# Performance work log

Hardware: AMD Instinct MI355X
Metric: run time of the kernel (lower is better)

Reference implementation:

```python
import jax, jax.numpy as jnp
import numpy as np

S = 4          # num_segments
T = 4096       # frames
D = 1024       # input_size == output_size
HEADS = 1
FREQ = 10000.0
DH = D // HEADS     # per-head width = 1024
TB = T // S         # block height = 1024
WB = DH // S        # block width  = 256


def _abs_pos(tb, d, freq):
    # Matches getAbsolutePosition: AP[p, 2i] = sin(p / freq^(2i/d)), AP[p, 2i+1] = cos(same).
    pos = jnp.arange(tb, dtype=jnp.float32)[:, None]          # [tb,1]
    i = jnp.arange(tb // 2, dtype=jnp.float32)[None, :]       # [1,tb//2]
    ang = pos / jnp.power(jnp.float32(freq), 2.0 * i / d)     # [tb,tb//2]
    ap = jnp.zeros((tb, tb), jnp.float32)
    return ap.at[:, 0::2].set(jnp.sin(ang)).at[:, 1::2].set(jnp.cos(ang))


def setup_inputs() -> dict:
    key = jax.random.key(0)
    ks = jax.random.split(key, 6)
    x = jax.random.normal(ks[0], (T, D), jnp.float32)
    Wq = jax.random.normal(ks[1], (HEADS, DH, D), jnp.float32) * 0.02
    Wk = jax.random.normal(ks[2], (HEADS, DH, D), jnp.float32) * 0.02
    Wv = jax.random.normal(ks[3], (HEADS, DH, D), jnp.float32) * 0.02
    Wout = jax.random.normal(ks[4], (D, D), jnp.float32) * 0.02
    Wout2 = jax.random.normal(ks[5], (WB, WB + 2), jnp.float32) * 0.05
    return {"x": x, "Wq": Wq, "Wk": Wk, "Wv": Wv, "Wout": Wout, "Wout2": Wout2}


def _forward(x, Wq, Wk, Wv, Wout, Wout2):
    # diversity = 1 - cosine similarity (F.normalize p=2 along dim=1)
    xu = x / jnp.maximum(jnp.linalg.norm(x, axis=1, keepdims=True), 1e-12)
    div = 1.0 - xu @ xu.T                                     # [T,T]

    Q = jnp.einsum('ti,hdi->htd', x, Wq)                      # [h,T,DH]
    K = jnp.einsum('ti,hdi->htd', x, Wk)
    V = jnp.einsum('ti,hdi->htd', x, Wv)

    def blk(A):  # [h,T,DH] -> [h,S*S,TB,WB], block (i,j) row-major as in local_x/local_y
        return A.reshape(-1, S, TB, S, WB).transpose(0, 1, 3, 2, 4).reshape(-1, S * S, TB, WB)

    qb, kb, vb = blk(Q), blk(K), blk(V)
    # diversity uses the diagonal row-block for every column-block j of row i
    drow = jnp.stack([div[i * TB:(i + 1) * TB, i * TB:(i + 1) * TB] for i in range(S)], 0)  # [S,TB,TB]
    db = jnp.repeat(drow, S, axis=0)[None]                    # [1,S*S,TB,TB]

    sim = jnp.einsum('hbqc,hbkc->hbqk', qb, kb) + _abs_pos(TB, D, FREQ)  # [h,S*S,TB,TB]
    attw = jax.nn.softmax(sim, axis=-1)
    # normalized row entropy, then L1-normalized (F.normalize p=1)
    ent = -(attw * jax.nn.log_softmax(sim, axis=-1)).sum(-1) / jnp.log(jnp.float32(TB))  # [h,S*S,TB]
    ent = ent / jnp.maximum(jnp.abs(ent).sum(-1, keepdims=True), 1e-12)

    dep = (db * attw).sum(-1) / db.sum(-1)                    # [h,S*S,TB]
    att_win = attw + dep[:, :, None, :] * attw                # dep_factor rows are identical
    ctx = jnp.einsum('hbqk,hbkc->hbqc', att_win, vb)          # [h,S*S,TB,WB]

    chars = jax.lax.stop_gradient(jnp.stack([ent, dep], axis=-1))  # [h,S*S,TB,2] (detach)
    y = jnp.concatenate([ctx, chars], axis=-1) @ Wout2.T      # [h,S*S,TB,WB]

    # reassemble grid of blocks back to [h,T,DH], concat heads, final projection
    y = y.reshape(-1, S, S, TB, WB).transpose(0, 1, 3, 2, 4).reshape(-1, T, DH)
    y = y.transpose(1, 0, 2).reshape(T, HEADS * DH)
    return y @ Wout.T                                         # [T,D]


def reference(x, Wq, Wk, Wv, Wout, Wout2):
    return _forward(x, Wq, Wk, Wv, Wout, Wout2)
```

## Files before the change

kernel.cpp:

```cpp
#include <hip/hip_runtime.h>
#include <hip/hip_bf16.h>

#define TT 4096
#define DD 1024
#define TBB 1024
#define WBB 256

typedef __attribute__((ext_vector_type(8))) _Float16 half8;
typedef __attribute__((ext_vector_type(4))) _Float16 half4;
typedef __attribute__((ext_vector_type(16))) float f32x16;

__device__ __forceinline__ unsigned short f2h(float v) {
  _Float16 h = (_Float16)v;
  return *reinterpret_cast<unsigned short*>(&h);
}
__device__ __forceinline__ float h2f(unsigned short u) {
  _Float16 h = *reinterpret_cast<_Float16*>(&u);
  return (float)h;
}

__device__ __forceinline__ void gl_lds16(const unsigned short* g, unsigned short* l) {
  __builtin_amdgcn_global_load_lds(
      (const __attribute__((address_space(1))) void*)(unsigned long long)(g),
      (__attribute__((address_space(3))) void*)(unsigned long long)(l),
      16, 0, 0);
}

__device__ __forceinline__ float waveSum(float v) {
#pragma unroll
  for (int o = 32; o > 0; o >>= 1) v += __shfl_down(v, o, 64);
  return v;
}
__device__ __forceinline__ float waveMax(float v) {
#pragma unroll
  for (int o = 32; o > 0; o >>= 1) v = fmaxf(v, __shfl_down(v, o, 64));
  return v;
}

template <int EPI, typename OutT>
__global__ __launch_bounds__(256) void gemm_bt(
    const unsigned short* __restrict__ A, const unsigned short* __restrict__ B,
    OutT* __restrict__ C,
    int K, int lda, int ldb, int ldc,
    int zbase, int zdiv,
    long sAi, long sAj, long sBi, long sBj, long sCi, long sCj,
    long sAz, long sBz, long sCz,
    const float* __restrict__ e0, const float* __restrict__ e1,
    const float* __restrict__ e2, const float* __restrict__ e3)
{
  __shared__ __align__(16) unsigned short lA[2][4096];
  __shared__ __align__(16) unsigned short lB[2][4096];

  const int z = blockIdx.z, gz = zbase + z;
  const int zi = gz / zdiv, zj = gz - zi * zdiv;
  const unsigned short* Ab = A + (long)zi * sAi + (long)zj * sAj + (long)z * sAz;
  const unsigned short* Bb = B + (long)zi * sBi + (long)zj * sBj + (long)z * sBz;
  const long offC = (long)zi * sCi + (long)zj * sCj + (long)z * sCz;

  const int m0 = blockIdx.y * 128, n0 = blockIdx.x * 128;
  const int tid = threadIdx.x, wave = tid >> 6, lane = tid & 63;
  const int wm = (wave >> 1) * 64, wn = (wave & 1) * 64;
  const int srow = lane >> 2;
  const int scol = (((lane & 3) ^ ((srow >> 1) & 3))) * 8;
  const int l31 = lane & 31, khi = lane >> 5;
  const int sw2 = (l31 >> 1) & 3;

  f32x16 acc[2][2] = {};

  for (int k0 = 0; k0 < K; k0 += 64) {
#pragma unroll
    for (int h = 0; h < 2; ++h)
#pragma unroll
      for (int t = 0; t < 2; ++t) {
        const int r = wave * 32 + t * 16 + srow;
        gl_lds16(Ab + (long)(m0 + r) * lda + (k0 + h * 32 + scol), &lA[h][wave * 1024 + t * 512]);
        gl_lds16(Bb + (long)(n0 + r) * ldb + (k0 + h * 32 + scol), &lB[h][wave * 1024 + t * 512]);
      }
    __syncthreads();

    half8 af[2][4], bfr[2][4];
#pragma unroll
    for (int mi = 0; mi < 2; ++mi)
#pragma unroll
      for (int ks = 0; ks < 4; ++ks)
        af[mi][ks] = *(const half8*)&lA[ks >> 1][(wm + mi * 32 + l31) * 32 + ((((ks & 1) * 2 + khi) ^ sw2) * 8)];
#pragma unroll
    for (int ni = 0; ni < 2; ++ni)
#pragma unroll
      for (int ks = 0; ks < 4; ++ks)
        bfr[ni][ks] = *(const half8*)&lB[ks >> 1][(wn + ni * 32 + l31) * 32 + ((((ks & 1) * 2 + khi) ^ sw2) * 8)];

#pragma unroll
    for (int ks = 0; ks < 4; ++ks)
#pragma unroll
      for (int mi = 0; mi < 2; ++mi)
#pragma unroll
        for (int ni = 0; ni < 2; ++ni)
          acc[mi][ni] = __builtin_amdgcn_mfma_f32_32x32x16_f16(af[mi][ks], bfr[ni][ks], acc[mi][ni], 0, 0, 0);
    __syncthreads();
  }

  OutT* Cb = C + offC;
#pragma unroll
  for (int mi = 0; mi < 2; ++mi)
#pragma unroll
    for (int ni = 0; ni < 2; ++ni)
#pragma unroll
      for (int r = 0; r < 16; ++r) {
        const int row = m0 + wm + mi * 32 + khi * 4 + (r & 3) + 8 * (r >> 2);
        const int col = n0 + wn + ni * 32 + l31;
        float v = acc[mi][ni][r];
        const long ci = (long)row * ldc + col;
        if constexpr (sizeof(OutT) == 2) {
          Cb[ci] = (OutT)f2h(v);
        } else {
          Cb[ci] = v;
        }
      }
}

template <int EPI, typename OutT>
__global__ __launch_bounds__(256) void gemm_s(
    const unsigned short* __restrict__ A, const unsigned short* __restrict__ B,
    OutT* __restrict__ C,
    int K, int lda, int ldb, int ldc,
    int zbase, int zdiv,
    long sAi, long sAj, long sBi, long sBj, long sCi, long sCj,
    long sAz, long sBz, long sCz,
    const float* __restrict__ e0, const float* __restrict__ e1,
    const float* __restrict__ e2, const float* __restrict__ e3)
{
  __shared__ __align__(16) unsigned short lA[2][2048];
  __shared__ __align__(16) unsigned short lB[2][2048];

  const int z = blockIdx.z, gz = zbase + z;
  const int zi = gz / zdiv, zj = gz - zi * zdiv;
  const unsigned short* Ab = A + (long)zi * sAi + (long)zj * sAj + (long)z * sAz;
  const unsigned short* Bb = B + (long)zi * sBi + (long)zj * sBj + (long)z * sBz;
  const long offC = (long)zi * sCi + (long)zj * sCj + (long)z * sCz;

  const int m0 = blockIdx.y * 64, n0 = blockIdx.x * 64;
  const int tid = threadIdx.x, wave = tid >> 6, lane = tid & 63;
  const int wm = (wave >> 1) * 32, wn = (wave & 1) * 32;
  const int srow = lane >> 2;
  const int grow = wave * 16 + srow;
  const int scol = (((lane & 3) ^ ((grow >> 1) & 3))) * 8;
  const int l31 = lane & 31, khi = lane >> 5;
  const int sw2 = (l31 >> 1) & 3;

  f32x16 acc = {};

  for (int k0 = 0; k0 < K; k0 += 64) {
#pragma unroll
    for (int h = 0; h < 2; ++h) {
      gl_lds16(Ab + (long)(m0 + grow) * lda + (k0 + h * 32 + scol), &lA[h][wave * 512]);
      gl_lds16(Bb + (long)(n0 + grow) * ldb + (k0 + h * 32 + scol), &lB[h][wave * 512]);
    }
    __syncthreads();

    half8 af[4], bfr[4];
#pragma unroll
    for (int ks = 0; ks < 4; ++ks) {
      af[ks] = *(const half8*)&lA[ks >> 1][(wm + l31) * 32 + ((((ks & 1) * 2 + khi) ^ sw2) * 8)];
      bfr[ks] = *(const half8*)&lB[ks >> 1][(wn + l31) * 32 + ((((ks & 1) * 2 + khi) ^ sw2) * 8)];
    }
#pragma unroll
    for (int ks = 0; ks < 4; ++ks)
      acc = __builtin_amdgcn_mfma_f32_32x32x16_f16(af[ks], bfr[ks], acc, 0, 0, 0);
    __syncthreads();
  }

  OutT* Cb = C + offC;
#pragma unroll
  for (int r = 0; r < 16; ++r) {
    const int row = m0 + wm + khi * 4 + (r & 3) + 8 * (r >> 2);
    const int col = n0 + wn + l31;
    float v = acc[r];
    if constexpr (EPI == 1) v = 1.0f - v;
    if constexpr (EPI == 3)
      v += e0[(long)gz * 1024 + row] * e2[col] + e1[(long)gz * 1024 + row] * e3[col];
    const long ci = (long)row * ldc + col;
    if constexpr (sizeof(OutT) == 2) {
      Cb[ci] = (OutT)f2h(v);
    } else {
      Cb[ci] = v;
    }
  }
}

__global__ __launch_bounds__(256) void sim_gemm(
    const unsigned short* __restrict__ A, const unsigned short* __restrict__ B,
    unsigned short* __restrict__ C,
    const unsigned short* __restrict__ APh)
{
  __shared__ __align__(16) unsigned short lA[2][4096];
  __shared__ __align__(16) unsigned short lB[2][4096];

  const int gz = blockIdx.z;
  const int zi = gz >> 2, zj = gz & 3;
  const unsigned short* Ab = A + (long)zi * (TBB * DD) + zj * WBB;
  const unsigned short* Bb = B + (long)zi * (TBB * DD) + zj * WBB;
  unsigned short* Cb = C + (long)gz * TBB * TBB;

  const int m0 = blockIdx.y * 128, n0 = blockIdx.x * 128;
  const int tid = threadIdx.x, wave = tid >> 6, lane = tid & 63;
  const int wm = (wave >> 1) * 64, wn = (wave & 1) * 64;
  const int srow = lane >> 2;
  const int scol = ((lane & 3) ^ ((srow >> 1) & 3)) * 8;
  const int l31 = lane & 31, khi = lane >> 5;
  const int sw2 = (l31 >> 1) & 3;

  f32x16 acc[2][2] = {};

  for (int k0 = 0; k0 < WBB; k0 += 64) {
#pragma unroll
    for (int h = 0; h < 2; ++h)
#pragma unroll
      for (int t = 0; t < 2; ++t) {
        const int r = wave * 32 + t * 16 + srow;
        gl_lds16(Ab + (long)(m0 + r) * DD + (k0 + h * 32 + scol), &lA[h][wave * 1024 + t * 512]);
        gl_lds16(Bb + (long)(n0 + r) * DD + (k0 + h * 32 + scol), &lB[h][wave * 1024 + t * 512]);
      }
    __syncthreads();

    half8 af[2][4], bfr[2][4];
#pragma unroll
    for (int mi = 0; mi < 2; ++mi)
#pragma unroll
      for (int ks = 0; ks < 4; ++ks)
        af[mi][ks] = *(const half8*)&lA[ks >> 1][(wm + mi * 32 + l31) * 32 + ((((ks & 1) * 2 + khi) ^ sw2) * 8)];
#pragma unroll
    for (int ni = 0; ni < 2; ++ni)
#pragma unroll
      for (int ks = 0; ks < 4; ++ks)
        bfr[ni][ks] = *(const half8*)&lB[ks >> 1][(wn + ni * 32 + l31) * 32 + ((((ks & 1) * 2 + khi) ^ sw2) * 8)];

#pragma unroll
    for (int ks = 0; ks < 4; ++ks)
#pragma unroll
      for (int mi = 0; mi < 2; ++mi)
#pragma unroll
        for (int ni = 0; ni < 2; ++ni)
          acc[mi][ni] = __builtin_amdgcn_mfma_f32_32x32x16_f16(af[mi][ks], bfr[ni][ks], acc[mi][ni], 0, 0, 0);
    __syncthreads();
  }

#pragma unroll
  for (int mi = 0; mi < 2; ++mi)
#pragma unroll
    for (int ni = 0; ni < 2; ++ni)
#pragma unroll
      for (int r = 0; r < 16; ++r) {
        const int row = m0 + wm + mi * 32 + khi * 4 + (r & 3) + 8 * (r >> 2);
        const int col = n0 + wn + ni * 32 + l31;
        Cb[(long)row * TBB + col] = f2h(acc[mi][ni][r] + h2f(APh[(long)row * 1024 + col]));
      }
}

__global__ __launch_bounds__(256) void ctx_gemm_s(
    const unsigned short* __restrict__ wpre, const float* __restrict__ dep,
    const unsigned short* __restrict__ Vt, unsigned short* __restrict__ ctx)
{
  __shared__ __align__(16) unsigned short lA[2][2048];
  __shared__ __align__(16) unsigned short lB[2][2048];
  __shared__ __align__(16) unsigned short sDepH[1024];

  const int gz = blockIdx.z, zi = gz >> 2, zj = gz & 3;
  const int m0 = blockIdx.y * 64, n0 = blockIdx.x * 64;
  const int tid = threadIdx.x, wave = tid >> 6, lane = tid & 63;
  const int wm = (wave >> 1) * 32, wn = (wave & 1) * 32;
  const int srow = lane >> 2;
  const int grow = wave * 16 + srow;
  const int scol = ((lane & 3) ^ ((grow >> 1) & 3)) * 8;
  const int l31 = lane & 31, khi = lane >> 5;
  const int sw2 = (l31 >> 1) & 3;

#pragma unroll
  for (int p = 0; p < 4; ++p)
    sDepH[tid + p * 256] = f2h(1.f + dep[(long)gz * 1024 + tid + p * 256]);
  __syncthreads();

  const unsigned short* Ab = wpre + (long)gz * TBB * TBB;
  const unsigned short* Bb = Vt + (long)(zj * 256) * TT + (long)zi * 1024;

  f32x16 acc = {};

  for (int k0 = 0; k0 < 1024; k0 += 64) {
#pragma unroll
    for (int h = 0; h < 2; ++h)
      gl_lds16(Bb + (long)(n0 + grow) * TT + (k0 + h * 32 + scol), &lB[h][wave * 512]);
#pragma unroll
    for (int h = 0; h < 2; ++h)
#pragma unroll
      for (int p = 0; p < 2; ++p) {
        const int idx = p * 1024 + tid * 4;
        const int row = idx >> 5, col = idx & 31;
        ushort4 wv = *(const ushort4*)(Ab + (long)(m0 + row) * 1024 + k0 + h * 32 + col);
        const half4 dv = *(const half4*)&sDepH[k0 + h * 32 + col];
        half4 pv = *(half4*)&wv * dv;
        const int pcol = (((col >> 3) ^ ((row >> 1) & 3)) << 3) | (col & 7);
        *(half4*)&lA[h][row * 32 + pcol] = pv;
      }
    __syncthreads();

    half8 af[4], bfr[4];
#pragma unroll
    for (int ks = 0; ks < 4; ++ks) {
      af[ks] = *(const half8*)&lA[ks >> 1][(wm + l31) * 32 + ((((ks & 1) * 2 + khi) ^ sw2) * 8)];
      bfr[ks] = *(const half8*)&lB[ks >> 1][(wn + l31) * 32 + ((((ks & 1) * 2 + khi) ^ sw2) * 8)];
    }
#pragma unroll
    for (int ks = 0; ks < 4; ++ks)
      acc = __builtin_amdgcn_mfma_f32_32x32x16_f16(af[ks], bfr[ks], acc, 0, 0, 0);
    __syncthreads();
  }

  unsigned short* Cb = ctx + (long)gz * TBB * WBB;
#pragma unroll
  for (int r = 0; r < 16; ++r) {
    const int row = m0 + wm + khi * 4 + (r & 3) + 8 * (r >> 2);
    const int col = n0 + wn + l31;
    Cb[(long)row * WBB + col] = f2h(acc[r]);
  }
}

__global__ __launch_bounds__(256) void prepx_kernel(
    const float* __restrict__ x, unsigned short* __restrict__ xh,
    unsigned short* __restrict__ xu)
{
  const int t = blockIdx.x, tid = threadIdx.x;
  const float4 v = *((const float4*)(x + (long)t * DD) + tid);
  float ss = v.x * v.x + v.y * v.y + v.z * v.z + v.w * v.w;
  ss = waveSum(ss);
  __shared__ float red[4];
  if ((tid & 63) == 0) red[tid >> 6] = ss;
  __syncthreads();
  const float tot = red[0] + red[1] + red[2] + red[3];
  const float inv = 1.f / fmaxf(sqrtf(tot), 1e-12f);
  ushort4 h, u;
  h.x = f2h(v.x); h.y = f2h(v.y); h.z = f2h(v.z); h.w = f2h(v.w);
  u.x = f2h(v.x * inv); u.y = f2h(v.y * inv); u.z = f2h(v.z * inv); u.w = f2h(v.w * inv);
  *((ushort4*)(xh + (long)t * DD) + tid) = h;
  *((ushort4*)(xu + (long)t * DD) + tid) = u;
}

__global__ __launch_bounds__(256) void castw_kernel(
    const float* __restrict__ Wq, const float* __restrict__ Wk, const float* __restrict__ Wv,
    unsigned short* __restrict__ o)
{
  const long idx4 = ((long)blockIdx.x * 256 + threadIdx.x) * 4;
  const int which = (int)(idx4 >> 20);
  const long loc = idx4 & ((1L << 20) - 1);
  const float* src = (which == 0) ? Wq : ((which == 1) ? Wk : Wv);
  const float4 v = *(const float4*)(src + loc);
  ushort4 h;
  h.x = f2h(v.x); h.y = f2h(v.y); h.z = f2h(v.z); h.w = f2h(v.w);
  *(ushort4*)(o + idx4) = h;
}

__global__ __launch_bounds__(256) void castp_kernel(const float* __restrict__ src,
                                                    unsigned short* __restrict__ dst)
{
  const long idx4 = ((long)blockIdx.x * 256 + threadIdx.x) * 4;
  const float4 v = *(const float4*)(src + idx4);
  ushort4 h;
  h.x = f2h(v.x); h.y = f2h(v.y); h.z = f2h(v.z); h.w = f2h(v.w);
  *(ushort4*)(dst + idx4) = h;
}

__global__ __launch_bounds__(256) void packw2_kernel(
    const float* __restrict__ W2, unsigned short* __restrict__ W2B,
    float* __restrict__ Ecol, float* __restrict__ Dcol)
{
  const int c = blockIdx.x, j = threadIdx.x;
  W2B[c * 256 + j] = f2h(W2[c * 258 + j]);
  if (j == 0) {
    Ecol[c] = W2[c * 258 + 256];
    Dcol[c] = W2[c * 258 + 257];
  }
}

__global__ __launch_bounds__(256) void ap_kernel(unsigned short* __restrict__ APh)
{
  const int p = blockIdx.x, tid = threadIdx.x;
#pragma unroll
  for (int t = 0; t < 4; ++t) {
    const int col = tid + t * 256;
    const int i = col >> 1;
    const float e = (2.0f * (float)i) / 1024.0f;
    const float ang = (float)p / powf(10000.0f, e);
    APh[(long)p * 1024 + col] = f2h((col & 1) ? cosf(ang) : sinf(ang));
  }
}

__global__ __launch_bounds__(256) void transpose_kernel(
    const unsigned short* __restrict__ V, unsigned short* __restrict__ Vt)
{
  __shared__ unsigned short tile[32][33];
  const int tx = threadIdx.x & 31, ty = threadIdx.x >> 5;
  const int c0 = blockIdx.x * 32;
  const int r0 = blockIdx.y * 32;
#pragma unroll
  for (int rr = ty; rr < 32; rr += 8)
    tile[rr][tx] = V[(long)(r0 + rr) * DD + c0 + tx];
  __syncthreads();
#pragma unroll
  for (int rr = ty; rr < 32; rr += 8)
    Vt[(long)(c0 + rr) * TT + r0 + tx] = tile[tx][rr];
}

__global__ __launch_bounds__(256) void stats_kernel(
    const unsigned short* __restrict__ sim, const unsigned short* __restrict__ divb,
    float* __restrict__ dep, float* __restrict__ ent,
    unsigned short* __restrict__ wpre)
{
  const int q = blockIdx.x, gz = blockIdx.y, bi = gz >> 2;
  const int tid = threadIdx.x;
  const unsigned short* srow = sim + ((long)gz * TBB + q) * TBB;
  const unsigned short* drow = divb + ((long)bi * TBB + q) * TBB;
  const ushort4 sv = ((const ushort4*)srow)[tid];
  const ushort4 dv = ((const ushort4*)drow)[tid];
  float s[4] = {h2f(sv.x), h2f(sv.y), h2f(sv.z), h2f(sv.w)};
  float d[4] = {h2f(dv.x), h2f(dv.y), h2f(dv.z), h2f(dv.w)};
  float m = fmaxf(fmaxf(s[0], s[1]), fmaxf(s[2], s[3]));
  m = waveMax(m);
  __shared__ float red[4];
  if ((tid & 63) == 0) red[tid >> 6] = m;
  __syncthreads();
  m = fmaxf(fmaxf(red[0], red[1]), fmaxf(red[2], red[3]));
  float e[4];
  float l = 0.f, ss = 0.f, dn = 0.f, ds = 0.f;
#pragma unroll
  for (int p = 0; p < 4; ++p) {
    e[p] = expf(s[p] - m);
    l += e[p]; ss += e[p] * s[p]; dn += e[p] * d[p]; ds += d[p];
  }
  l = waveSum(l); ss = waveSum(ss); dn = waveSum(dn); ds = waveSum(ds);
  __shared__ float r2[16];
  if ((tid & 63) == 0) {
    const int w = tid >> 6;
    r2[w] = l; r2[4 + w] = ss; r2[8 + w] = dn; r2[12 + w] = ds;
  }
  __syncthreads();
  const float L = r2[0] + r2[1] + r2[2] + r2[3];
  const float Li = 1.f / L;
  ushort4 wq;
  wq.x = f2h(e[0] * Li); wq.y = f2h(e[1] * Li);
  wq.z = f2h(e[2] * Li); wq.w = f2h(e[3] * Li);
  ((ushort4*)(wpre + ((long)gz * TBB + q) * TBB))[tid] = wq;
  if (tid == 0) {
    const float SS = r2[4] + r2[5] + r2[6] + r2[7];
    const float DN = r2[8] + r2[9] + r2[10] + r2[11];
    const float DS = r2[12] + r2[13] + r2[14] + r2[15];
    const long o = (long)gz * TBB + q;
    dep[o] = (DN * Li) / DS;
    ent[o] = (m + logf(L) - SS * Li) * 0.14426950408889634f;
  }
}

__global__ __launch_bounds__(256) void entnorm_kernel(float* __restrict__ ent)
{
  const int gz = blockIdx.x, tid = threadIdx.x;
  float s = 0.f;
#pragma unroll
  for (int p = 0; p < 4; ++p) s += fabsf(ent[(long)gz * TBB + tid + p * 256]);
  s = waveSum(s);
  __shared__ float red[4];
  if ((tid & 63) == 0) red[tid >> 6] = s;
  __syncthreads();
  const float scale = 1.f / fmaxf(red[0] + red[1] + red[2] + red[3], 1e-12f);
#pragma unroll
  for (int p = 0; p < 4; ++p) ent[(long)gz * TBB + tid + p * 256] *= scale;
}

extern "C" void kernel_launch(void* const* d_in, const int* in_sizes, int n_in,
                              void* d_out, int out_size, void* d_ws, size_t ws_size,
                              hipStream_t stream)
{
  const float* x  = (const float*)d_in[0];
  const float* Wq = (const float*)d_in[1];
  const float* Wk = (const float*)d_in[2];
  const float* Wv = (const float*)d_in[3];
  const float* Wo = (const float*)d_in[4];
  const float* W2 = (const float*)d_in[5];

  char* ws = (char*)d_ws;
  size_t off = 0;
  auto take = [&](size_t bytes) -> void* {
    void* p = ws + off;
    off += (bytes + 255) & ~(size_t)255;
    return p;
  };
  unsigned short* QKV = (unsigned short*)take((size_t)3 * TT * DD * 2);
  unsigned short* xh  = (unsigned short*)take((size_t)TT * DD * 2);
  unsigned short* xu  = (unsigned short*)take((size_t)TT * DD * 2);
  unsigned short* Wh  = (unsigned short*)take((size_t)3 * DD * DD * 2);
  unsigned short* WoB = (unsigned short*)take((size_t)DD * DD * 2);
  unsigned short* W2B = (unsigned short*)take((size_t)256 * 256 * 2);
  float* Ecol = (float*)take(256 * 4);
  float* Dcol = (float*)take(256 * 4);
  unsigned short* APh = (unsigned short*)take((size_t)TBB * TBB * 2);
  unsigned short* divb = (unsigned short*)take((size_t)4 * TBB * TBB * 2);
  unsigned short* Vt = (unsigned short*)take((size_t)DD * TT * 2);
  unsigned short* simh = (unsigned short*)take((size_t)16 * TBB * TBB * 2);
  unsigned short* wpre = (unsigned short*)take((size_t)16 * TBB * TBB * 2);
  float* depb = (float*)take((size_t)16 * TBB * 4);
  float* entb = (float*)take((size_t)16 * TBB * 4);
  unsigned short* ctx = (unsigned short*)take((size_t)16 * TBB * WBB * 2);
  unsigned short* Y = (unsigned short*)take((size_t)TT * DD * 2);
  (void)ws_size; (void)in_sizes; (void)n_in; (void)out_size;

  prepx_kernel<<<TT, 256, 0, stream>>>(x, xh, xu);
  castw_kernel<<<(3 * DD * DD) / 1024, 256, 0, stream>>>(Wq, Wk, Wv, Wh);
  castp_kernel<<<(DD * DD) / 1024, 256, 0, stream>>>(Wo, WoB);
  packw2_kernel<<<256, 256, 0, stream>>>(W2, W2B, Ecol, Dcol);
  ap_kernel<<<TBB, 256, 0, stream>>>(APh);

  gemm_bt<0, unsigned short><<<dim3(DD / 128, TT / 128, 3), 256, 0, stream>>>(
      xh, Wh, QKV,
      DD, DD, DD, DD, 0, 1,
      0, 0, (long)DD * DD, 0, (long)TT * DD, 0,
      0, 0, 0, nullptr, nullptr, nullptr, nullptr);

  transpose_kernel<<<dim3(DD / 32, TT / 32), 256, 0, stream>>>(QKV + (size_t)2 * TT * DD, Vt);

  gemm_s<1, unsigned short><<<dim3(16, 16, 4), 256, 0, stream>>>(
      xu, xu, divb,
      DD, DD, DD, TBB, 0, 1,
      (long)TBB * DD, 0, (long)TBB * DD, 0, (long)TBB * TBB, 0,
      0, 0, 0, nullptr, nullptr, nullptr, nullptr);

  const unsigned short* Qh = QKV;
  const unsigned short* Kh = QKV + (size_t)TT * DD;

  sim_gemm<<<dim3(8, 8, 16), 256, 0, stream>>>(Qh, Kh, simh, APh);

  stats_kernel<<<dim3(TBB, 16), 256, 0, stream>>>(simh, divb, depb, entb, wpre);
  entnorm_kernel<<<16, 256, 0, stream>>>(entb);

  ctx_gemm_s<<<dim3(4, 16, 16), 256, 0, stream>>>(wpre, depb, Vt, ctx);

  gemm_s<3, unsigned short><<<dim3(4, 16, 16), 256, 0, stream>>>(
      ctx, W2B, Y,
      WBB, WBB, WBB, DD, 0, 4,
      (long)4 * TBB * WBB, (long)TBB * WBB, 0, 0, (long)TBB * DD, (long)WBB,
      0, 0, 0, entb, depb, Ecol, Dcol);

  gemm_s<0, float><<<dim3(16, 64, 1), 256, 0, stream>>>(
      Y, WoB, (float*)d_out,
      DD, DD, DD, DD, 0, 1,
      0, 0, 0, 0, 0, 0,
      0, 0, 0, nullptr, nullptr, nullptr, nullptr);
}
```

Baseline: 271.4 us.

## Recompute softmax probabilities in ctx GEMM and fold entropy normalization into stats

The stats kernel stops writing a normalized fp16 probability matrix. It now writes a per-row log-sum-exp offset, and the context GEMM recomputes exp(sim - B) while loading its A tile. This removes a 32 MB write and its later re-read, at the cost of extra exp work inside the GEMM prologue. The stats kernel is also reworked to handle one row per wave with xor shuffles and no shared memory. The entropy L1 normalization kernel is dropped: sums are accumulated by atomics and the scale is applied in the Wout2 epilogue. Separately, the two weight-cast kernels are merged into one.

```diff
diff --git a/kernel.cpp b/kernel.cpp
--- a/kernel.cpp
+++ b/kernel.cpp
@@ -31,9 +31,14 @@
   for (int o = 32; o > 0; o >>= 1) v += __shfl_down(v, o, 64);
   return v;
 }
-__device__ __forceinline__ float waveMax(float v) {
-#pragma unroll
-  for (int o = 32; o > 0; o >>= 1) v = fmaxf(v, __shfl_down(v, o, 64));
+__device__ __forceinline__ float bSum(float v) {
+#pragma unroll
+  for (int o = 32; o > 0; o >>= 1) v += __shfl_xor(v, o, 64);
+  return v;
+}
+__device__ __forceinline__ float bMax(float v) {
+#pragma unroll
+  for (int o = 32; o > 0; o >>= 1) v = fmaxf(v, __shfl_xor(v, o, 64));
   return v;
 }
 
@@ -46,7 +51,8 @@
     long sAi, long sAj, long sBi, long sBj, long sCi, long sCj,
     long sAz, long sBz, long sCz,
     const float* __restrict__ e0, const float* __restrict__ e1,
-    const float* __restrict__ e2, const float* __restrict__ e3)
+    const float* __restrict__ e2, const float* __restrict__ e3,
+    const float* __restrict__ e4)
 {
   __shared__ __align__(16) unsigned short lA[2][4096];
   __shared__ __align__(16) unsigned short lB[2][4096];
@@ -128,7 +134,8 @@
     long sAi, long sAj, long sBi, long sBj, long sCi, long sCj,
     long sAz, long sBz, long sCz,
     const float* __restrict__ e0, const float* __restrict__ e1,
-    const float* __restrict__ e2, const float* __restrict__ e3)
+    const float* __restrict__ e2, const float* __restrict__ e3,
+    const float* __restrict__ e4)
 {
   __shared__ __align__(16) unsigned short lA[2][2048];
   __shared__ __align__(16) unsigned short lB[2][2048];
@@ -148,6 +155,9 @@
   const int l31 = lane & 31, khi = lane >> 5;
   const int sw2 = (l31 >> 1) & 3;
 
+  float esc = 0.f;
+  if constexpr (EPI == 3) esc = 1.f / fmaxf(e4[gz], 1e-12f);
+
   f32x16 acc = {};
 
   for (int k0 = 0; k0 < K; k0 += 64) {
@@ -178,7 +188,7 @@
     float v = acc[r];
     if constexpr (EPI == 1) v = 1.0f - v;
     if constexpr (EPI == 3)
-      v += e0[(long)gz * 1024 + row] * e2[col] + e1[(long)gz * 1024 + row] * e3[col];
+      v += e0[(long)gz * 1024 + row] * esc * e2[col] + e1[(long)gz * 1024 + row] * e3[col];
     const long ci = (long)row * ldc + col;
     if constexpr (sizeof(OutT) == 2) {
       Cb[ci] = (OutT)f2h(v);
@@ -258,7 +268,8 @@
 }
 
 __global__ __launch_bounds__(256) void ctx_gemm_s(
-    const unsigned short* __restrict__ wpre, const float* __restrict__ dep,
+    const unsigned short* __restrict__ simh, const float* __restrict__ dep,
+    const float* __restrict__ Brow,
     const unsigned short* __restrict__ Vt, unsigned short* __restrict__ ctx)
 {
   __shared__ __align__(16) unsigned short lA[2][2048];
@@ -280,7 +291,10 @@
     sDepH[tid + p * 256] = f2h(1.f + dep[(long)gz * 1024 + tid + p * 256]);
   __syncthreads();
 
-  const unsigned short* Ab = wpre + (long)gz * TBB * TBB;
+  const float B0 = Brow[(long)gz * 1024 + m0 + (tid >> 3)];
+  const float B1 = Brow[(long)gz * 1024 + m0 + 32 + (tid >> 3)];
+
+  const unsigned short* Ab = simh + (long)gz * TBB * TBB;
   const unsigned short* Bb = Vt + (long)(zj * 256) * TT + (long)zi * 1024;
 
   f32x16 acc = {};
@@ -295,9 +309,15 @@
       for (int p = 0; p < 2; ++p) {
         const int idx = p * 1024 + tid * 4;
         const int row = idx >> 5, col = idx & 31;
-        ushort4 wv = *(const ushort4*)(Ab + (long)(m0 + row) * 1024 + k0 + h * 32 + col);
+        const ushort4 wv = *(const ushort4*)(Ab + (long)(m0 + row) * 1024 + k0 + h * 32 + col);
+        const float Bp = p ? B1 : B0;
+        half4 ev;
+        ev.x = (_Float16)exp2f(fmaf(h2f(wv.x), 1.4426950408889634f, -Bp));
+        ev.y = (_Float16)exp2f(fmaf(h2f(wv.y), 1.4426950408889634f, -Bp));
+        ev.z = (_Float16)exp2f(fmaf(h2f(wv.z), 1.4426950408889634f, -Bp));
+        ev.w = (_Float16)exp2f(fmaf(h2f(wv.w), 1.4426950408889634f, -Bp));
         const half4 dv = *(const half4*)&sDepH[k0 + h * 32 + col];
-        half4 pv = *(half4*)&wv * dv;
+        half4 pv = ev * dv;
         const int pcol = (((col >> 3) ^ ((row >> 1) & 3)) << 3) | (col & 7);
         *(half4*)&lA[h][row * 32 + pcol] = pv;
       }
@@ -344,33 +364,26 @@
   *((ushort4*)(xu + (long)t * DD) + tid) = u;
 }
 
-__global__ __launch_bounds__(256) void castw_kernel(
-    const float* __restrict__ Wq, const float* __restrict__ Wk, const float* __restrict__ Wv,
-    unsigned short* __restrict__ o)
+__global__ __launch_bounds__(256) void castall_kernel(
+    const float* __restrict__ Wq, const float* __restrict__ Wk,
+    const float* __restrict__ Wv, const float* __restrict__ Wo,
+    unsigned short* __restrict__ Wh, unsigned short* __restrict__ WoB)
 {
   const long idx4 = ((long)blockIdx.x * 256 + threadIdx.x) * 4;
   const int which = (int)(idx4 >> 20);
   const long loc = idx4 & ((1L << 20) - 1);
-  const float* src = (which == 0) ? Wq : ((which == 1) ? Wk : Wv);
+  const float* src = (which == 0) ? Wq : ((which == 1) ? Wk : ((which == 2) ? Wv : Wo));
+  unsigned short* dst = (which < 3) ? (Wh + idx4) : (WoB + loc);
   const float4 v = *(const float4*)(src + loc);
   ushort4 h;
   h.x = f2h(v.x); h.y = f2h(v.y); h.z = f2h(v.z); h.w = f2h(v.w);
-  *(ushort4*)(o + idx4) = h;
-}
-
-__global__ __launch_bounds__(256) void castp_kernel(const float* __restrict__ src,
-                                                    unsigned short* __restrict__ dst)
-{
-  const long idx4 = ((long)blockIdx.x * 256 + threadIdx.x) * 4;
-  const float4 v = *(const float4*)(src + idx4);
-  ushort4 h;
-  h.x = f2h(v.x); h.y = f2h(v.y); h.z = f2h(v.z); h.w = f2h(v.w);
-  *(ushort4*)(dst + idx4) = h;
+  *(ushort4*)dst = h;
 }
 
 __global__ __launch_bounds__(256) void packw2_kernel(
     const float* __restrict__ W2, unsigned short* __restrict__ W2B,
-    float* __restrict__ Ecol, float* __restrict__ Dcol)
+    float* __restrict__ Ecol, float* __restrict__ Dcol,
+    float* __restrict__ entsum)
 {
   const int c = blockIdx.x, j = threadIdx.x;
   W2B[c * 256 + j] = f2h(W2[c * 258 + j]);
@@ -378,6 +391,7 @@
     Ecol[c] = W2[c * 258 + 256];
     Dcol[c] = W2[c * 258 + 257];
   }
+  if (c == 0 && j < 16) entsum[j] = 0.f;
 }
 
 __global__ __launch_bounds__(256) void ap_kernel(unsigned short* __restrict__ APh)
@@ -388,7 +402,7 @@
     const int col = tid + t * 256;
     const int i = col >> 1;
     const float e = (2.0f * (float)i) / 1024.0f;
-    const float ang = (float)p / powf(10000.0f, e);
+    const float ang = (float)p * exp2f(e * -13.287712379549449f);
     APh[(long)p * 1024 + col] = f2h((col & 1) ? cosf(ang) : sinf(ang));
   }
 }
@@ -412,65 +426,45 @@
 __global__ __launch_bounds__(256) void stats_kernel(
     const unsigned short* __restrict__ sim, const unsigned short* __restrict__ divb,
     float* __restrict__ dep, float* __restrict__ ent,
-    unsigned short* __restrict__ wpre)
-{
-  const int q = blockIdx.x, gz = blockIdx.y, bi = gz >> 2;
-  const int tid = threadIdx.x;
+    float* __restrict__ Brow, float* __restrict__ entsum)
+{
+  const int gz = blockIdx.y, bi = gz >> 2;
+  const int wave = threadIdx.x >> 6, lane = threadIdx.x & 63;
+  const int q = blockIdx.x * 4 + wave;
   const unsigned short* srow = sim + ((long)gz * TBB + q) * TBB;
   const unsigned short* drow = divb + ((long)bi * TBB + q) * TBB;
-  const ushort4 sv = ((const ushort4*)srow)[tid];
-  const ushort4 dv = ((const ushort4*)drow)[tid];
-  float s[4] = {h2f(sv.x), h2f(sv.y), h2f(sv.z), h2f(sv.w)};
-  float d[4] = {h2f(dv.x), h2f(dv.y), h2f(dv.z), h2f(dv.w)};
-  float m = fmaxf(fmaxf(s[0], s[1]), fmaxf(s[2], s[3]));
-  m = waveMax(m);
-  __shared__ float red[4];
-  if ((tid & 63) == 0) red[tid >> 6] = m;
-  __syncthreads();
-  m = fmaxf(fmaxf(red[0], red[1]), fmaxf(red[2], red[3]));
-  float e[4];
+  float s[16], d[16];
+#pragma unroll
+  for (int u = 0; u < 4; ++u) {
+    const ushort4 sv = *(const ushort4*)(srow + u * 256 + lane * 4);
+    const ushort4 dv = *(const ushort4*)(drow + u * 256 + lane * 4);
+    s[u * 4 + 0] = h2f(sv.x); s[u * 4 + 1] = h2f(sv.y);
+    s[u * 4 + 2] = h2f(sv.z); s[u * 4 + 3] = h2f(sv.w);
+    d[u * 4 + 0] = h2f(dv.x); d[u * 4 + 1] = h2f(dv.y);
+    d[u * 4 + 2] = h2f(dv.z); d[u * 4 + 3] = h2f(dv.w);
+  }
+  float m = s[0];
+#pragma unroll
+  for (int i = 1; i < 16; ++i) m = fmaxf(m, s[i]);
+  m = bMax(m);
+  const float mB = m * 1.4426950408889634f;
   float l = 0.f, ss = 0.f, dn = 0.f, ds = 0.f;
 #pragma unroll
-  for (int p = 0; p < 4; ++p) {
-    e[p] = expf(s[p] - m);
-    l += e[p]; ss += e[p] * s[p]; dn += e[p] * d[p]; ds += d[p];
-  }
-  l = waveSum(l); ss = waveSum(ss); dn = waveSum(dn); ds = waveSum(ds);
-  __shared__ float r2[16];
-  if ((tid & 63) == 0) {
-    const int w = tid >> 6;
-    r2[w] = l; r2[4 + w] = ss; r2[8 + w] = dn; r2[12 + w] = ds;
-  }
-  __syncthreads();
-  const float L = r2[0] + r2[1] + r2[2] + r2[3];
-  const float Li = 1.f / L;
-  ushort4 wq;
-  wq.x = f2h(e[0] * Li); wq.y = f2h(e[1] * Li);
-  wq.z = f2h(e[2] * Li); wq.w = f2h(e[3] * Li);
-  ((ushort4*)(wpre + ((long)gz * TBB + q) * TBB))[tid] = wq;
-  if (tid == 0) {
-    const float SS = r2[4] + r2[5] + r2[6] + r2[7];
-    const float DN = r2[8] + r2[9] + r2[10] + r2[11];
-    const float DS = r2[12] + r2[13] + r2[14] + r2[15];
+  for (int i = 0; i < 16; ++i) {
+    const float e = exp2f(fmaf(s[i], 1.4426950408889634f, -mB));
+    l += e; ss += e * s[i]; dn += e * d[i]; ds += d[i];
+  }
+  l = bSum(l); ss = bSum(ss); dn = bSum(dn); ds = bSum(ds);
+  if (lane == 0) {
     const long o = (long)gz * TBB + q;
-    dep[o] = (DN * Li) / DS;
-    ent[o] = (m + logf(L) - SS * Li) * 0.14426950408889634f;
-  }
-}
-
-__global__ __launch_bounds__(256) void entnorm_kernel(float* __restrict__ ent)
-{
-  const int gz = blockIdx.x, tid = threadIdx.x;
-  float s = 0.f;
-#pragma unroll
-  for (int p = 0; p < 4; ++p) s += fabsf(ent[(long)gz * TBB + tid + p * 256]);
-  s = waveSum(s);
-  __shared__ float red[4];
-  if ((tid & 63) == 0) red[tid >> 6] = s;
-  __syncthreads();
-  const float scale = 1.f / fmaxf(red[0] + red[1] + red[2] + red[3], 1e-12f);
-#pragma unroll
-  for (int p = 0; p < 4; ++p) ent[(long)gz * TBB + tid + p * 256] *= scale;
+    const float Li = 1.f / l;
+    const float lnL = logf(l);
+    dep[o] = (dn * Li) / ds;
+    const float entv = (m + lnL - ss * Li) * 0.14426950408889634f;
+    ent[o] = entv;
+    Brow[o] = (m + lnL) * 1.4426950408889634f;
+    atomicAdd(&entsum[gz], fabsf(entv));
+  }
 }
 
 extern "C" void kernel_launch(void* const* d_in, const int* in_sizes, int n_in,
@@ -503,24 +497,24 @@
   unsigned short* divb = (unsigned short*)take((size_t)4 * TBB * TBB * 2);
   unsigned short* Vt = (unsigned short*)take((size_t)DD * TT * 2);
   unsigned short* simh = (unsigned short*)take((size_t)16 * TBB * TBB * 2);
-  unsigned short* wpre = (unsigned short*)take((size_t)16 * TBB * TBB * 2);
   float* depb = (float*)take((size_t)16 * TBB * 4);
   float* entb = (float*)take((size_t)16 * TBB * 4);
+  float* Brow = (float*)take((size_t)16 * TBB * 4);
+  float* entsum = (float*)take((size_t)16 * 4);
   unsigned short* ctx = (unsigned short*)take((size_t)16 * TBB * WBB * 2);
   unsigned short* Y = (unsigned short*)take((size_t)TT * DD * 2);
   (void)ws_size; (void)in_sizes; (void)n_in; (void)out_size;
 
   prepx_kernel<<<TT, 256, 0, stream>>>(x, xh, xu);
-  castw_kernel<<<(3 * DD * DD) / 1024, 256, 0, stream>>>(Wq, Wk, Wv, Wh);
-  castp_kernel<<<(DD * DD) / 1024, 256, 0, stream>>>(Wo, WoB);
-  packw2_kernel<<<256, 256, 0, stream>>>(W2, W2B, Ecol, Dcol);
+  castall_kernel<<<(4 * DD * DD) / 1024, 256, 0, stream>>>(Wq, Wk, Wv, Wo, Wh, WoB);
+  packw2_kernel<<<256, 256, 0, stream>>>(W2, W2B, Ecol, Dcol, entsum);
   ap_kernel<<<TBB, 256, 0, stream>>>(APh);
 
   gemm_bt<0, unsigned short><<<dim3(DD / 128, TT / 128, 3), 256, 0, stream>>>(
       xh, Wh, QKV,
       DD, DD, DD, DD, 0, 1,
       0, 0, (long)DD * DD, 0, (long)TT * DD, 0,
-      0, 0, 0, nullptr, nullptr, nullptr, nullptr);
+      0, 0, 0, nullptr, nullptr, nullptr, nullptr, nullptr);
 
   transpose_kernel<<<dim3(DD / 32, TT / 32), 256, 0, stream>>>(QKV + (size_t)2 * TT * DD, Vt);
 
@@ -528,27 +522,26 @@
       xu, xu, divb,
       DD, DD, DD, TBB, 0, 1,
       (long)TBB * DD, 0, (long)TBB * DD, 0, (long)TBB * TBB, 0,
-      0, 0, 0, nullptr, nullptr, nullptr, nullptr);
+      0, 0, 0, nullptr, nullptr, nullptr, nullptr, nullptr);
 
   const unsigned short* Qh = QKV;
   const unsigned short* Kh = QKV + (size_t)TT * DD;
 
   sim_gemm<<<dim3(8, 8, 16), 256, 0, stream>>>(Qh, Kh, simh, APh);
 
-  stats_kernel<<<dim3(TBB, 16), 256, 0, stream>>>(simh, divb, depb, entb, wpre);
-  entnorm_kernel<<<16, 256, 0, stream>>>(entb);
-
-  ctx_gemm_s<<<dim3(4, 16, 16), 256, 0, stream>>>(wpre, depb, Vt, ctx);
+  stats_kernel<<<dim3(TBB / 4, 16), 256, 0, stream>>>(simh, divb, depb, entb, Brow, entsum);
+
+  ctx_gemm_s<<<dim3(4, 16, 16), 256, 0, stream>>>(simh, depb, Brow, Vt, ctx);
 
   gemm_s<3, unsigned short><<<dim3(4, 16, 16), 256, 0, stream>>>(
       ctx, W2B, Y,
       WBB, WBB, WBB, DD, 0, 4,
       (long)4 * TBB * WBB, (long)TBB * WBB, 0, 0, (long)TBB * DD, (long)WBB,
-      0, 0, 0, entb, depb, Ecol, Dcol);
+      0, 0, 0, entb, depb, Ecol, Dcol, entsum);
 
   gemm_s<0, float><<<dim3(16, 64, 1), 256, 0, stream>>>(
       Y, WoB, (float*)d_out,
       DD, DD, DD, DD, 0, 1,
       0, 0, 0, 0, 0, 0,
-      0, 0, 0, nullptr, nullptr, nullptr, nullptr);
-}
+      0, 0, 0, nullptr, nullptr, nullptr, nullptr, nullptr);
+}
```

After: 455.2 us. 67.7% more time.
